# Optimization experiments

Measured on AMD Instinct MI355X. Metric: run time of the kernel, lower is better.

Reference implementation:

```python
import jax, jax.numpy as jnp
import numpy as np

B, S, D = 8, 1024, 1024
H, DH = 16, 64  # n_heads, d_head; D == H*DH


def setup_inputs() -> dict:
    key = jax.random.key(0)
    ks = jax.random.split(key, 7)
    scale = 1.0 / np.sqrt(DH)
    return {
        "images": jax.random.normal(ks[0], (B, S, D), dtype=jnp.float32),
        "Wq": jax.random.normal(ks[1], (H, DH, DH), dtype=jnp.float32) * scale,
        "bq": jax.random.normal(ks[2], (H, DH), dtype=jnp.float32) * scale,
        "Wk": jax.random.normal(ks[3], (H, DH, DH), dtype=jnp.float32) * scale,
        "bk": jax.random.normal(ks[4], (H, DH), dtype=jnp.float32) * scale,
        "Wv": jax.random.normal(ks[5], (H, DH, DH), dtype=jnp.float32) * scale,
        "bv": jax.random.normal(ks[6], (H, DH), dtype=jnp.float32) * scale,
    }


def reference(images, Wq, bq, Wk, bk, Wv, bv):
    Bn, Sn, Dn = images.shape
    x = images.reshape(Bn, Sn, H, DH)  # split hidden dim into per-head slices
    # torch Linear: y = x @ W.T + b, per head -> einsum over input dim d
    q = jnp.einsum("bshd,hod->bsho", x, Wq) + bq  # [B,S,H,DH]
    k = jnp.einsum("bshd,hod->bsho", x, Wk) + bk
    v = jnp.einsum("bshd,hod->bsho", x, Wv) + bv
    scores = jnp.einsum("bqhd,bkhd->bhqk", q, k) / jnp.sqrt(jnp.asarray(DH, x.dtype))
    attn = jax.nn.softmax(scores, axis=-1)  # [B,H,S,S]
    out = jnp.einsum("bhqk,bkhd->bqhd", attn, v)  # [B,S,H,DH]
    return out.reshape(Bn, Sn, Dn)  # hstack across heads == reshape back
```

## Files before the change

kernel.cpp:

```cpp
#include <hip/hip_runtime.h>
#include <hip/hip_bf16.h>

#define B_ 8
#define S_ 1024
#define D_ 1024
#define H_ 16
#define DH_ 64

typedef __attribute__((ext_vector_type(8))) short short8;
typedef __attribute__((ext_vector_type(8))) unsigned short ushort8;
typedef __attribute__((ext_vector_type(4))) unsigned short us4;
typedef __attribute__((ext_vector_type(4))) unsigned int uint4v;
typedef __attribute__((ext_vector_type(4))) float f32x4;

#define QSCALE 0.18033688011112042f

static __device__ __forceinline__ unsigned short f2bf(float f) {
    union { float f; unsigned u; } v; v.f = f;
    unsigned r = v.u + 0x7fffu + ((v.u >> 16) & 1u);
    return (unsigned short)(r >> 16);
}

static __device__ __forceinline__ void stage8(const float* __restrict__ src, unsigned short* dst) {
    float4 a = *reinterpret_cast<const float4*>(src);
    float4 b = *reinterpret_cast<const float4*>(src + 4);
    ushort8 r;
    r[0] = f2bf(a.x); r[1] = f2bf(a.y); r[2] = f2bf(a.z); r[3] = f2bf(a.w);
    r[4] = f2bf(b.x); r[5] = f2bf(b.y); r[6] = f2bf(b.z); r[7] = f2bf(b.w);
    *reinterpret_cast<ushort8*>(dst) = r;
}

static __device__ __forceinline__ unsigned int cvtpk(float a, float b) {
    unsigned int r;
    asm("v_cvt_pk_bf16_f32 %0, %1, %2" : "=v"(r) : "v"(a), "v"(b));
    return r;
}

__global__ __launch_bounds__(256) void qkv_proj(
    const float* __restrict__ x,
    const float* __restrict__ Wq, const float* __restrict__ bq,
    const float* __restrict__ Wk, const float* __restrict__ bk,
    const float* __restrict__ Wv, const float* __restrict__ bv,
    unsigned short* __restrict__ qo, unsigned short* __restrict__ ko,
    unsigned short* __restrict__ vo)
{
    const int bid   = blockIdx.x;
    const int stile = bid & 15;
    const int h     = (bid >> 4) & (H_ - 1);
    const int b     = bid >> 8;
    const int tid   = threadIdx.x;
    const int lane  = tid & 63;
    const int wave  = tid >> 6;
    const int lr    = lane & 15;
    const int lk    = lane >> 4;

    __shared__ __align__(16) unsigned short xs[64][72];
    __shared__ __align__(16) unsigned short wsh[3][64][72];

    {
        int row = tid >> 2;
        int col = (tid & 3) * 16;
        const float* src = x + ((size_t)(b * S_ + stile * 64 + row)) * D_ + h * DH_ + col;
        stage8(src,     &xs[row][col]);
        stage8(src + 8, &xs[row][col + 8]);
        const float* wsrc[3] = { Wq + h * DH_ * DH_, Wk + h * DH_ * DH_, Wv + h * DH_ * DH_ };
        #pragma unroll
        for (int p = 0; p < 3; ++p) {
            const float* s = wsrc[p] + row * DH_ + col;
            stage8(s,     &wsh[p][row][col]);
            stage8(s + 8, &wsh[p][row][col + 8]);
        }
    }
    __syncthreads();

    short8 a[2];
    #pragma unroll
    for (int kk = 0; kk < 2; ++kk)
        a[kk] = *reinterpret_cast<const short8*>(&xs[wave * 16 + lr][8 * lk + 32 * kk]);

    f32x4 acc[3][4];
    #pragma unroll
    for (int p = 0; p < 3; ++p)
        #pragma unroll
        for (int n = 0; n < 4; ++n)
            acc[p][n] = (f32x4){0.f, 0.f, 0.f, 0.f};

    #pragma unroll
    for (int p = 0; p < 3; ++p)
        #pragma unroll
        for (int kk = 0; kk < 2; ++kk)
            #pragma unroll
            for (int n = 0; n < 4; ++n) {
                short8 bf = *reinterpret_cast<const short8*>(&wsh[p][lr + 16 * n][8 * lk + 32 * kk]);
                acc[p][n] = __builtin_amdgcn_mfma_f32_16x16x32_bf16(a[kk], bf, acc[p][n], 0, 0, 0);
            }

    size_t base = ((size_t)(b * H_ + h) * S_ + stile * 64 + wave * 16) * DH_;
    #pragma unroll
    for (int p = 0; p < 2; ++p) {
        const float* bias = p ? (bk + h * DH_) : (bq + h * DH_);
        unsigned short* op = p ? ko : qo;
        #pragma unroll
        for (int n = 0; n < 4; ++n) {
            int col = lr + 16 * n;
            float bb = bias[col];
            #pragma unroll
            for (int r = 0; r < 4; ++r) {
                float val = acc[p][n][r] + bb;
                if (p == 0) val *= QSCALE;
                op[base + (size_t)(4 * lk + r) * DH_ + col] = f2bf(val);
            }
        }
    }
    {
        size_t vbase = (size_t)(b * H_ + h) * DH_ * S_;
        int s0 = stile * 64 + wave * 16 + 4 * lk;
        #pragma unroll
        for (int n = 0; n < 4; ++n) {
            int dh = lr + 16 * n;
            float bb = bv[h * DH_ + dh];
            us4 w;
            #pragma unroll
            for (int r = 0; r < 4; ++r) w[r] = f2bf(acc[2][n][r] + bb);
            *reinterpret_cast<us4*>(vo + vbase + (size_t)dh * S_ + s0) = w;
        }
    }
}

__global__ __launch_bounds__(256, 4) void attn_fwd(
    const unsigned short* __restrict__ q,
    const unsigned short* __restrict__ k,
    const unsigned short* __restrict__ vt,
    float* __restrict__ out)
{
    const int bid   = (blockIdx.x & 7) * 128 + (blockIdx.x >> 3);
    const int qtile = bid & 7;
    const int h     = (bid >> 3) & (H_ - 1);
    const int b     = bid >> 7;
    const int tid   = threadIdx.x;
    const int lane  = tid & 63;
    const int wave  = tid >> 6;
    const int lr    = lane & 15;
    const int lk    = lane >> 4;

    __shared__ __align__(16) unsigned short ks[2][64][64];
    __shared__ __align__(16) unsigned short vs[2][64][64];

    const size_t bh = (size_t)(b * H_ + h) * S_ * DH_;

    short8 qf[2][2];
    #pragma unroll
    for (int g = 0; g < 2; ++g) {
        const unsigned short* qp = q + bh + (size_t)(qtile * 128 + wave * 32 + 16 * g + lr) * DH_;
        #pragma unroll
        for (int kk = 0; kk < 2; ++kk)
            qf[g][kk] = *reinterpret_cast<const short8*>(qp + 8 * lk + 32 * kk);
    }

    const int srow = tid >> 2;
    const int c0   = (tid & 3) * 2;
    const int prow = (srow & 0x23) | ((srow & 4) << 2) | ((srow & 0x18) >> 1);
    const int kx   = prow & 7, vx = srow & 7;
    ushort8 kreg[2], vreg[2];

    {
        const unsigned short* srck = k + bh + (size_t)srow * DH_ + c0 * 8;
        kreg[0] = *reinterpret_cast<const ushort8*>(srck);
        kreg[1] = *reinterpret_cast<const ushort8*>(srck + 8);
        const unsigned short* srcv = vt + bh + (size_t)srow * S_ + c0 * 8;
        vreg[0] = *reinterpret_cast<const ushort8*>(srcv);
        vreg[1] = *reinterpret_cast<const ushort8*>(srcv + 8);
        *reinterpret_cast<ushort8*>(&ks[0][prow][(c0 ^ kx) * 8])       = kreg[0];
        *reinterpret_cast<ushort8*>(&ks[0][prow][((c0 + 1) ^ kx) * 8]) = kreg[1];
        *reinterpret_cast<ushort8*>(&vs[0][srow][(c0 ^ vx) * 8])       = vreg[0];
        *reinterpret_cast<ushort8*>(&vs[0][srow][((c0 + 1) ^ vx) * 8]) = vreg[1];
    }

    f32x4 acc[2][4];
    #pragma unroll
    for (int g = 0; g < 2; ++g)
        #pragma unroll
        for (int n = 0; n < 4; ++n) acc[g][n] = (f32x4){0.f, 0.f, 0.f, 0.f};
    float l0 = 0.f, l1 = 0.f;

    const int rx = lr & 7;
    const int NT = S_ / 64;
    for (int t = 0; t < NT; ++t) {
        __syncthreads();

        if (t + 1 < NT) {
            const unsigned short* srck = k + bh + (size_t)((t + 1) * 64 + srow) * DH_ + c0 * 8;
            kreg[0] = *reinterpret_cast<const ushort8*>(srck);
            kreg[1] = *reinterpret_cast<const ushort8*>(srck + 8);
            const unsigned short* srcv = vt + bh + (size_t)srow * S_ + (t + 1) * 64 + c0 * 8;
            vreg[0] = *reinterpret_cast<const ushort8*>(srcv);
            vreg[1] = *reinterpret_cast<const ushort8*>(srcv + 8);
        }
        const int cur = t & 1;

        f32x4 st[2][4];
        #pragma unroll
        for (int g = 0; g < 2; ++g)
            #pragma unroll
            for (int n = 0; n < 4; ++n) st[g][n] = (f32x4){0.f, 0.f, 0.f, 0.f};
        #pragma unroll
        for (int kk = 0; kk < 2; ++kk)
            #pragma unroll
            for (int n = 0; n < 4; ++n) {
                short8 ka = *reinterpret_cast<const short8*>(
                    &ks[cur][16 * n + lr][((lk + 4 * kk) ^ rx) * 8]);
                st[0][n] = __builtin_amdgcn_mfma_f32_16x16x32_bf16(ka, qf[0][kk], st[0][n], 0, 0, 0);
                st[1][n] = __builtin_amdgcn_mfma_f32_16x16x32_bf16(ka, qf[1][kk], st[1][n], 0, 0, 0);
            }

        #pragma unroll
        for (int g = 0; g < 2; ++g)
            #pragma unroll
            for (int n = 0; n < 4; ++n)
                #pragma unroll
                for (int r = 0; r < 4; ++r)
                    st[g][n][r] = __builtin_amdgcn_exp2f(st[g][n][r]);
        {
            float a0 = (st[0][0][0] + st[0][0][1]) + (st[0][0][2] + st[0][0][3]);
            float a1 = (st[0][1][0] + st[0][1][1]) + (st[0][1][2] + st[0][1][3]);
            float a2 = (st[0][2][0] + st[0][2][1]) + (st[0][2][2] + st[0][2][3]);
            float a3 = (st[0][3][0] + st[0][3][1]) + (st[0][3][2] + st[0][3][3]);
            l0 += (a0 + a1) + (a2 + a3);
            float b0 = (st[1][0][0] + st[1][0][1]) + (st[1][0][2] + st[1][0][3]);
            float b1 = (st[1][1][0] + st[1][1][1]) + (st[1][1][2] + st[1][1][3]);
            float b2 = (st[1][2][0] + st[1][2][1]) + (st[1][2][2] + st[1][2][3]);
            float b3 = (st[1][3][0] + st[1][3][1]) + (st[1][3][2] + st[1][3][3]);
            l1 += (b0 + b1) + (b2 + b3);
        }

        short8 pa[2][2];
        #pragma unroll
        for (int g = 0; g < 2; ++g)
            #pragma unroll
            for (int kk = 0; kk < 2; ++kk) {
                uint4v w4;
                w4[0] = cvtpk(st[g][2 * kk][0],     st[g][2 * kk][1]);
                w4[1] = cvtpk(st[g][2 * kk][2],     st[g][2 * kk][3]);
                w4[2] = cvtpk(st[g][2 * kk + 1][0], st[g][2 * kk + 1][1]);
                w4[3] = cvtpk(st[g][2 * kk + 1][2], st[g][2 * kk + 1][3]);
                pa[g][kk] = __builtin_bit_cast(short8, w4);
            }

        #pragma unroll
        for (int kk = 0; kk < 2; ++kk)
            #pragma unroll
            for (int n = 0; n < 4; ++n) {
                short8 va = *reinterpret_cast<const short8*>(
                    &vs[cur][16 * n + lr][((lk + 4 * kk) ^ rx) * 8]);
                acc[0][n] = __builtin_amdgcn_mfma_f32_16x16x32_bf16(va, pa[0][kk], acc[0][n], 0, 0, 0);
                acc[1][n] = __builtin_amdgcn_mfma_f32_16x16x32_bf16(va, pa[1][kk], acc[1][n], 0, 0, 0);
            }

        if (t + 1 < NT) {
            const int nxt = cur ^ 1;
            *reinterpret_cast<ushort8*>(&ks[nxt][prow][(c0 ^ kx) * 8])       = kreg[0];
            *reinterpret_cast<ushort8*>(&ks[nxt][prow][((c0 + 1) ^ kx) * 8]) = kreg[1];
            *reinterpret_cast<ushort8*>(&vs[nxt][srow][(c0 ^ vx) * 8])       = vreg[0];
            *reinterpret_cast<ushort8*>(&vs[nxt][srow][((c0 + 1) ^ vx) * 8]) = vreg[1];
        }
    }

    l0 += __shfl_xor(l0, 16, 64); l0 += __shfl_xor(l0, 32, 64);
    l1 += __shfl_xor(l1, 16, 64); l1 += __shfl_xor(l1, 32, 64);
    const float inv0 = 1.f / l0, inv1 = 1.f / l1;
    #pragma unroll
    for (int g = 0; g < 2; ++g) {
        const float inv = g ? inv1 : inv0;
        const int qrow = qtile * 128 + wave * 32 + 16 * g + lr;
        float* op = out + (size_t)(b * S_ + qrow) * D_ + h * DH_;
        #pragma unroll
        for (int n = 0; n < 4; ++n) {
            float4 o;
            o.x = acc[g][n][0] * inv; o.y = acc[g][n][1] * inv;
            o.z = acc[g][n][2] * inv; o.w = acc[g][n][3] * inv;
            *reinterpret_cast<float4*>(op + 16 * n + 4 * lk) = o;
        }
    }
}

extern "C" void kernel_launch(void* const* d_in, const int* in_sizes, int n_in,
                              void* d_out, int out_size, void* d_ws, size_t ws_size,
                              hipStream_t stream) {
    const float* x  = (const float*)d_in[0];
    const float* Wq = (const float*)d_in[1];
    const float* bq = (const float*)d_in[2];
    const float* Wk = (const float*)d_in[3];
    const float* bk = (const float*)d_in[4];
    const float* Wv = (const float*)d_in[5];
    const float* bv = (const float*)d_in[6];
    float* out = (float*)d_out;

    unsigned short* qw = (unsigned short*)d_ws;
    size_t per = (size_t)B_ * H_ * S_ * DH_;
    unsigned short* kw = qw + per;
    unsigned short* vw = kw + per;

    qkv_proj<<<dim3(B_ * H_ * (S_ / 64)), 256, 0, stream>>>(x, Wq, bq, Wk, bk, Wv, bv, qw, kw, vw);
    attn_fwd<<<dim3(B_ * H_ * (S_ / 128)), 256, 0, stream>>>(qw, kw, vw, out);
}
```

Baseline: 68.82 us.

## Enlarge attention query tile and stage K/V via direct global-to-LDS loads

Each attention block now processes 256 query rows, with 64 rows per wave instead of 32. Every K/V tile loaded into LDS therefore feeds twice as many MFMAs, and the grid is halved. The register-staged K/V prefetch is replaced by global_load_lds DMA into the double buffer, with the swizzle applied on the global source address rather than the LDS destination. In exchange, register pressure roughly doubles for accumulators and scores, and occupancy drops (launch bounds 256,2 with only 512 blocks), so there is less latency hiding.

```diff
diff --git a/kernel.cpp b/kernel.cpp
--- a/kernel.cpp
+++ b/kernel.cpp
@@ -34,6 +34,13 @@
     unsigned int r;
     asm("v_cvt_pk_bf16_f32 %0, %1, %2" : "=v"(r) : "v"(a), "v"(b));
     return r;
+}
+
+static __device__ __forceinline__ void gll16(const void* g, void* l) {
+    __builtin_amdgcn_global_load_lds(
+        (const __attribute__((address_space(1))) unsigned int*)g,
+        (__attribute__((address_space(3))) unsigned int*)l,
+        16, 0, 0);
 }
 
 __global__ __launch_bounds__(256) void qkv_proj(
@@ -127,16 +134,16 @@
     }
 }
 
-__global__ __launch_bounds__(256, 4) void attn_fwd(
+__global__ __launch_bounds__(256, 2) void attn_fwd(
     const unsigned short* __restrict__ q,
     const unsigned short* __restrict__ k,
     const unsigned short* __restrict__ vt,
     float* __restrict__ out)
 {
-    const int bid   = (blockIdx.x & 7) * 128 + (blockIdx.x >> 3);
-    const int qtile = bid & 7;
-    const int h     = (bid >> 3) & (H_ - 1);
-    const int b     = bid >> 7;
+    const int bid   = (blockIdx.x & 7) * 64 + (blockIdx.x >> 3);
+    const int qtile = bid & 3;
+    const int h     = (bid >> 2) & (H_ - 1);
+    const int b     = bid >> 6;
     const int tid   = threadIdx.x;
     const int lane  = tid & 63;
     const int wave  = tid >> 6;
@@ -148,59 +155,58 @@
 
     const size_t bh = (size_t)(b * H_ + h) * S_ * DH_;
 
-    short8 qf[2][2];
-    #pragma unroll
-    for (int g = 0; g < 2; ++g) {
-        const unsigned short* qp = q + bh + (size_t)(qtile * 128 + wave * 32 + 16 * g + lr) * DH_;
+    short8 qf[4][2];
+    #pragma unroll
+    for (int g = 0; g < 4; ++g) {
+        const unsigned short* qp = q + bh + (size_t)(qtile * 256 + wave * 64 + 16 * g + lr) * DH_;
         #pragma unroll
         for (int kk = 0; kk < 2; ++kk)
             qf[g][kk] = *reinterpret_cast<const short8*>(qp + 8 * lk + 32 * kk);
     }
 
-    const int srow = tid >> 2;
-    const int c0   = (tid & 3) * 2;
-    const int prow = (srow & 0x23) | ((srow & 4) << 2) | ((srow & 0x18) >> 1);
-    const int kx   = prow & 7, vx = srow & 7;
-    ushort8 kreg[2], vreg[2];
-
-    {
-        const unsigned short* srck = k + bh + (size_t)srow * DH_ + c0 * 8;
-        kreg[0] = *reinterpret_cast<const ushort8*>(srck);
-        kreg[1] = *reinterpret_cast<const ushort8*>(srck + 8);
-        const unsigned short* srcv = vt + bh + (size_t)srow * S_ + c0 * 8;
-        vreg[0] = *reinterpret_cast<const ushort8*>(srcv);
-        vreg[1] = *reinterpret_cast<const ushort8*>(srcv + 8);
-        *reinterpret_cast<ushort8*>(&ks[0][prow][(c0 ^ kx) * 8])       = kreg[0];
-        *reinterpret_cast<ushort8*>(&ks[0][prow][((c0 + 1) ^ kx) * 8]) = kreg[1];
-        *reinterpret_cast<ushort8*>(&vs[0][srow][(c0 ^ vx) * 8])       = vreg[0];
-        *reinterpret_cast<ushort8*>(&vs[0][srow][((c0 + 1) ^ vx) * 8]) = vreg[1];
-    }
-
-    f32x4 acc[2][4];
-    #pragma unroll
-    for (int g = 0; g < 2; ++g)
+    const int rp0 = 16 * wave + (lane >> 3);
+    const int rp1 = rp0 + 8;
+    const int c   = lane & 7;
+    const int gk0 = (rp0 & 0x23) | ((rp0 & 0x10) >> 2) | ((rp0 & 0x0C) << 1);
+    const int gk1 = (rp1 & 0x23) | ((rp1 & 0x10) >> 2) | ((rp1 & 0x0C) << 1);
+    const size_t kofs0 = (size_t)gk0 * DH_ + (c ^ (rp0 & 7)) * 8;
+    const size_t kofs1 = (size_t)gk1 * DH_ + (c ^ (rp1 & 7)) * 8;
+    const size_t vofs0 = (size_t)rp0 * S_ + (c ^ (rp0 & 7)) * 8;
+    const size_t vofs1 = (size_t)rp1 * S_ + (c ^ (rp1 & 7)) * 8;
+    const unsigned short* kb = k + bh;
+    const unsigned short* vb = vt + bh;
+
+    gll16(kb + kofs0, &ks[0][16 * wave][0]);
+    gll16(kb + kofs1, &ks[0][16 * wave + 8][0]);
+    gll16(vb + vofs0, &vs[0][16 * wave][0]);
+    gll16(vb + vofs1, &vs[0][16 * wave + 8][0]);
+
+    f32x4 acc[4][4];
+    #pragma unroll
+    for (int g = 0; g < 4; ++g)
         #pragma unroll
         for (int n = 0; n < 4; ++n) acc[g][n] = (f32x4){0.f, 0.f, 0.f, 0.f};
-    float l0 = 0.f, l1 = 0.f;
+    float l[4] = {0.f, 0.f, 0.f, 0.f};
 
     const int rx = lr & 7;
     const int NT = S_ / 64;
     for (int t = 0; t < NT; ++t) {
         __syncthreads();
+        const int cur = t & 1;
 
         if (t + 1 < NT) {
-            const unsigned short* srck = k + bh + (size_t)((t + 1) * 64 + srow) * DH_ + c0 * 8;
-            kreg[0] = *reinterpret_cast<const ushort8*>(srck);
-            kreg[1] = *reinterpret_cast<const ushort8*>(srck + 8);
-            const unsigned short* srcv = vt + bh + (size_t)srow * S_ + (t + 1) * 64 + c0 * 8;
-            vreg[0] = *reinterpret_cast<const ushort8*>(srcv);
-            vreg[1] = *reinterpret_cast<const ushort8*>(srcv + 8);
-        }
-        const int cur = t & 1;
-
-        f32x4 st[2][4];
-        #pragma unroll
-        for (int g = 0; g < 2; ++g)
+            const int nxt = cur ^ 1;
+            const unsigned short* kt = kb + (size_t)(t + 1) * 64 * DH_;
+            const unsigned short* vtb = vb + (size_t)(t + 1) * 64;
+            gll16(kt + kofs0, &ks[nxt][16 * wave][0]);
+            gll16(kt + kofs1, &ks[nxt][16 * wave + 8][0]);
+            gll16(vtb + vofs0, &vs[nxt][16 * wave][0]);
+            gll16(vtb + vofs1, &vs[nxt][16 * wave + 8][0]);
+        }
+
+        f32x4 st[4][4];
+        #pragma unroll
+        for (int g = 0; g < 4; ++g)
             #pragma unroll
             for (int n = 0; n < 4; ++n) st[g][n] = (f32x4){0.f, 0.f, 0.f, 0.f};
         #pragma unroll
@@ -209,33 +215,28 @@
             for (int n = 0; n < 4; ++n) {
                 short8 ka = *reinterpret_cast<const short8*>(
                     &ks[cur][16 * n + lr][((lk + 4 * kk) ^ rx) * 8]);
-                st[0][n] = __builtin_amdgcn_mfma_f32_16x16x32_bf16(ka, qf[0][kk], st[0][n], 0, 0, 0);
-                st[1][n] = __builtin_amdgcn_mfma_f32_16x16x32_bf16(ka, qf[1][kk], st[1][n], 0, 0, 0);
-            }
-
-        #pragma unroll
-        for (int g = 0; g < 2; ++g)
+                #pragma unroll
+                for (int g = 0; g < 4; ++g)
+                    st[g][n] = __builtin_amdgcn_mfma_f32_16x16x32_bf16(ka, qf[g][kk], st[g][n], 0, 0, 0);
+            }
+
+        #pragma unroll
+        for (int g = 0; g < 4; ++g) {
             #pragma unroll
             for (int n = 0; n < 4; ++n)
                 #pragma unroll
                 for (int r = 0; r < 4; ++r)
                     st[g][n][r] = __builtin_amdgcn_exp2f(st[g][n][r]);
-        {
-            float a0 = (st[0][0][0] + st[0][0][1]) + (st[0][0][2] + st[0][0][3]);
-            float a1 = (st[0][1][0] + st[0][1][1]) + (st[0][1][2] + st[0][1][3]);
-            float a2 = (st[0][2][0] + st[0][2][1]) + (st[0][2][2] + st[0][2][3]);
-            float a3 = (st[0][3][0] + st[0][3][1]) + (st[0][3][2] + st[0][3][3]);
-            l0 += (a0 + a1) + (a2 + a3);
-            float b0 = (st[1][0][0] + st[1][0][1]) + (st[1][0][2] + st[1][0][3]);
-            float b1 = (st[1][1][0] + st[1][1][1]) + (st[1][1][2] + st[1][1][3]);
-            float b2 = (st[1][2][0] + st[1][2][1]) + (st[1][2][2] + st[1][2][3]);
-            float b3 = (st[1][3][0] + st[1][3][1]) + (st[1][3][2] + st[1][3][3]);
-            l1 += (b0 + b1) + (b2 + b3);
-        }
-
-        short8 pa[2][2];
-        #pragma unroll
-        for (int g = 0; g < 2; ++g)
+            float a0 = (st[g][0][0] + st[g][0][1]) + (st[g][0][2] + st[g][0][3]);
+            float a1 = (st[g][1][0] + st[g][1][1]) + (st[g][1][2] + st[g][1][3]);
+            float a2 = (st[g][2][0] + st[g][2][1]) + (st[g][2][2] + st[g][2][3]);
+            float a3 = (st[g][3][0] + st[g][3][1]) + (st[g][3][2] + st[g][3][3]);
+            l[g] += (a0 + a1) + (a2 + a3);
+        }
+
+        short8 pa[4][2];
+        #pragma unroll
+        for (int g = 0; g < 4; ++g)
             #pragma unroll
             for (int kk = 0; kk < 2; ++kk) {
                 uint4v w4;
@@ -252,26 +253,19 @@
             for (int n = 0; n < 4; ++n) {
                 short8 va = *reinterpret_cast<const short8*>(
                     &vs[cur][16 * n + lr][((lk + 4 * kk) ^ rx) * 8]);
-                acc[0][n] = __builtin_amdgcn_mfma_f32_16x16x32_bf16(va, pa[0][kk], acc[0][n], 0, 0, 0);
-                acc[1][n] = __builtin_amdgcn_mfma_f32_16x16x32_bf16(va, pa[1][kk], acc[1][n], 0, 0, 0);
-            }
-
-        if (t + 1 < NT) {
-            const int nxt = cur ^ 1;
-            *reinterpret_cast<ushort8*>(&ks[nxt][prow][(c0 ^ kx) * 8])       = kreg[0];
-            *reinterpret_cast<ushort8*>(&ks[nxt][prow][((c0 + 1) ^ kx) * 8]) = kreg[1];
-            *reinterpret_cast<ushort8*>(&vs[nxt][srow][(c0 ^ vx) * 8])       = vreg[0];
-            *reinterpret_cast<ushort8*>(&vs[nxt][srow][((c0 + 1) ^ vx) * 8]) = vreg[1];
-        }
-    }
-
-    l0 += __shfl_xor(l0, 16, 64); l0 += __shfl_xor(l0, 32, 64);
-    l1 += __shfl_xor(l1, 16, 64); l1 += __shfl_xor(l1, 32, 64);
-    const float inv0 = 1.f / l0, inv1 = 1.f / l1;
-    #pragma unroll
-    for (int g = 0; g < 2; ++g) {
-        const float inv = g ? inv1 : inv0;
-        const int qrow = qtile * 128 + wave * 32 + 16 * g + lr;
+                #pragma unroll
+                for (int g = 0; g < 4; ++g)
+                    acc[g][n] = __builtin_amdgcn_mfma_f32_16x16x32_bf16(va, pa[g][kk], acc[g][n], 0, 0, 0);
+            }
+    }
+
+    #pragma unroll
+    for (int g = 0; g < 4; ++g) {
+        float lg = l[g];
+        lg += __shfl_xor(lg, 16, 64);
+        lg += __shfl_xor(lg, 32, 64);
+        const float inv = 1.f / lg;
+        const int qrow = qtile * 256 + wave * 64 + 16 * g + lr;
         float* op = out + (size_t)(b * S_ + qrow) * D_ + h * DH_;
         #pragma unroll
         for (int n = 0; n < 4; ++n) {
@@ -301,5 +295,5 @@
     unsigned short* vw = kw + per;
 
     qkv_proj<<<dim3(B_ * H_ * (S_ / 64)), 256, 0, stream>>>(x, Wq, bq, Wk, bk, Wv, bv, qw, kw, vw);
-    attn_fwd<<<dim3(B_ * H_ * (S_ / 128)), 256, 0, stream>>>(qw, kw, vw, out);
-}
+    attn_fwd<<<dim3(B_ * H_ * (S_ / 256)), 256, 0, stream>>>(qw, kw, vw, out);
+}
```

Result: faster. 66.60 us (-3.2%).

## Stage K/V tiles via global_load_lds with 128-key tiles

Applied to the files above, without the earlier changes.

Replaces the register-staged global-to-LDS copy of K and V tiles with direct global_load_lds DMA, applying the XOR swizzle on the global side. It also doubles the key tile from 64 to 128, which halves the number of loop iterations and barriers. Launch bounds drop to 2 blocks per CU because LDS and register use grow. The intent is to remove VGPR staging and LDS store instructions and to overlap the next tile's load with compute. The cost is lower occupancy and a prefetch that has no explicit wait before the barrier, which could be a correctness risk.

```diff
diff --git a/kernel.cpp b/kernel.cpp
--- a/kernel.cpp
+++ b/kernel.cpp
@@ -34,6 +34,13 @@
     unsigned int r;
     asm("v_cvt_pk_bf16_f32 %0, %1, %2" : "=v"(r) : "v"(a), "v"(b));
     return r;
+}
+
+static __device__ __forceinline__ void gll16(const void* g, void* l) {
+    __builtin_amdgcn_global_load_lds(
+        (const __attribute__((address_space(1))) unsigned int*)g,
+        (__attribute__((address_space(3))) unsigned int*)l,
+        16, 0, 0);
 }
 
 __global__ __launch_bounds__(256) void qkv_proj(
@@ -127,7 +134,7 @@
     }
 }
 
-__global__ __launch_bounds__(256, 4) void attn_fwd(
+__global__ __launch_bounds__(256, 2) void attn_fwd(
     const unsigned short* __restrict__ q,
     const unsigned short* __restrict__ k,
     const unsigned short* __restrict__ vt,
@@ -143,8 +150,8 @@
     const int lr    = lane & 15;
     const int lk    = lane >> 4;
 
-    __shared__ __align__(16) unsigned short ks[2][64][64];
-    __shared__ __align__(16) unsigned short vs[2][64][64];
+    __shared__ __align__(16) unsigned short ks[2][128][64];
+    __shared__ __align__(16) unsigned short vs[2][64][128];
 
     const size_t bh = (size_t)(b * H_ + h) * S_ * DH_;
 
@@ -157,23 +164,22 @@
             qf[g][kk] = *reinterpret_cast<const short8*>(qp + 8 * lk + 32 * kk);
     }
 
-    const int srow = tid >> 2;
-    const int c0   = (tid & 3) * 2;
-    const int prow = (srow & 0x23) | ((srow & 4) << 2) | ((srow & 0x18) >> 1);
-    const int kx   = prow & 7, vx = srow & 7;
-    ushort8 kreg[2], vreg[2];
-
-    {
-        const unsigned short* srck = k + bh + (size_t)srow * DH_ + c0 * 8;
-        kreg[0] = *reinterpret_cast<const ushort8*>(srck);
-        kreg[1] = *reinterpret_cast<const ushort8*>(srck + 8);
-        const unsigned short* srcv = vt + bh + (size_t)srow * S_ + c0 * 8;
-        vreg[0] = *reinterpret_cast<const ushort8*>(srcv);
-        vreg[1] = *reinterpret_cast<const ushort8*>(srcv + 8);
-        *reinterpret_cast<ushort8*>(&ks[0][prow][(c0 ^ kx) * 8])       = kreg[0];
-        *reinterpret_cast<ushort8*>(&ks[0][prow][((c0 + 1) ^ kx) * 8]) = kreg[1];
-        *reinterpret_cast<ushort8*>(&vs[0][srow][(c0 ^ vx) * 8])       = vreg[0];
-        *reinterpret_cast<ushort8*>(&vs[0][srow][((c0 + 1) ^ vx) * 8]) = vreg[1];
+    size_t kofs[4], vofs[4];
+    #pragma unroll
+    for (int j = 0; j < 4; ++j) {
+        const int rp = 32 * wave + 8 * j + (lane >> 3);
+        const int gk = (rp & 0x63) | ((rp & 0x10) >> 2) | ((rp & 0x0C) << 1);
+        kofs[j] = (size_t)gk * DH_ + (size_t)(((lane & 7) ^ (rp & 7)) * 8);
+        const int rv = 16 * wave + 4 * j + (lane >> 4);
+        vofs[j] = (size_t)rv * S_ + (size_t)(((lane & 15) ^ (rv & 15)) * 8);
+    }
+    const unsigned short* kb = k + bh;
+    const unsigned short* vb = vt + bh;
+
+    #pragma unroll
+    for (int j = 0; j < 4; ++j) {
+        gll16(kb + kofs[j], &ks[0][32 * wave + 8 * j][0]);
+        gll16(vb + vofs[j], &vs[0][16 * wave + 4 * j][0]);
     }
 
     f32x4 acc[2][4];
@@ -181,32 +187,34 @@
     for (int g = 0; g < 2; ++g)
         #pragma unroll
         for (int n = 0; n < 4; ++n) acc[g][n] = (f32x4){0.f, 0.f, 0.f, 0.f};
-    float l0 = 0.f, l1 = 0.f;
+    float l[2] = {0.f, 0.f};
 
     const int rx = lr & 7;
-    const int NT = S_ / 64;
+    const int NT = S_ / 128;
     for (int t = 0; t < NT; ++t) {
         __syncthreads();
+        const int cur = t & 1;
 
         if (t + 1 < NT) {
-            const unsigned short* srck = k + bh + (size_t)((t + 1) * 64 + srow) * DH_ + c0 * 8;
-            kreg[0] = *reinterpret_cast<const ushort8*>(srck);
-            kreg[1] = *reinterpret_cast<const ushort8*>(srck + 8);
-            const unsigned short* srcv = vt + bh + (size_t)srow * S_ + (t + 1) * 64 + c0 * 8;
-            vreg[0] = *reinterpret_cast<const ushort8*>(srcv);
-            vreg[1] = *reinterpret_cast<const ushort8*>(srcv + 8);
-        }
-        const int cur = t & 1;
-
-        f32x4 st[2][4];
+            const int nxt = cur ^ 1;
+            const unsigned short* kt  = kb + (size_t)(t + 1) * 128 * DH_;
+            const unsigned short* vtb = vb + (size_t)(t + 1) * 128;
+            #pragma unroll
+            for (int j = 0; j < 4; ++j) {
+                gll16(kt + kofs[j],  &ks[nxt][32 * wave + 8 * j][0]);
+                gll16(vtb + vofs[j], &vs[nxt][16 * wave + 4 * j][0]);
+            }
+        }
+
+        f32x4 st[2][8];
         #pragma unroll
         for (int g = 0; g < 2; ++g)
             #pragma unroll
-            for (int n = 0; n < 4; ++n) st[g][n] = (f32x4){0.f, 0.f, 0.f, 0.f};
+            for (int n = 0; n < 8; ++n) st[g][n] = (f32x4){0.f, 0.f, 0.f, 0.f};
         #pragma unroll
         for (int kk = 0; kk < 2; ++kk)
             #pragma unroll
-            for (int n = 0; n < 4; ++n) {
+            for (int n = 0; n < 8; ++n) {
                 short8 ka = *reinterpret_cast<const short8*>(
                     &ks[cur][16 * n + lr][((lk + 4 * kk) ^ rx) * 8]);
                 st[0][n] = __builtin_amdgcn_mfma_f32_16x16x32_bf16(ka, qf[0][kk], st[0][n], 0, 0, 0);
@@ -214,30 +222,26 @@
             }
 
         #pragma unroll
-        for (int g = 0; g < 2; ++g)
-            #pragma unroll
-            for (int n = 0; n < 4; ++n)
+        for (int g = 0; g < 2; ++g) {
+            #pragma unroll
+            for (int n = 0; n < 8; ++n)
                 #pragma unroll
                 for (int r = 0; r < 4; ++r)
                     st[g][n][r] = __builtin_amdgcn_exp2f(st[g][n][r]);
-        {
-            float a0 = (st[0][0][0] + st[0][0][1]) + (st[0][0][2] + st[0][0][3]);
-            float a1 = (st[0][1][0] + st[0][1][1]) + (st[0][1][2] + st[0][1][3]);
-            float a2 = (st[0][2][0] + st[0][2][1]) + (st[0][2][2] + st[0][2][3]);
-            float a3 = (st[0][3][0] + st[0][3][1]) + (st[0][3][2] + st[0][3][3]);
-            l0 += (a0 + a1) + (a2 + a3);
-            float b0 = (st[1][0][0] + st[1][0][1]) + (st[1][0][2] + st[1][0][3]);
-            float b1 = (st[1][1][0] + st[1][1][1]) + (st[1][1][2] + st[1][1][3]);
-            float b2 = (st[1][2][0] + st[1][2][1]) + (st[1][2][2] + st[1][2][3]);
-            float b3 = (st[1][3][0] + st[1][3][1]) + (st[1][3][2] + st[1][3][3]);
-            l1 += (b0 + b1) + (b2 + b3);
-        }
-
-        short8 pa[2][2];
+            float s0 = 0.f, s1 = 0.f;
+            #pragma unroll
+            for (int n = 0; n < 4; ++n) {
+                s0 += (st[g][n][0] + st[g][n][1]) + (st[g][n][2] + st[g][n][3]);
+                s1 += (st[g][n + 4][0] + st[g][n + 4][1]) + (st[g][n + 4][2] + st[g][n + 4][3]);
+            }
+            l[g] += s0 + s1;
+        }
+
+        short8 pa[2][4];
         #pragma unroll
         for (int g = 0; g < 2; ++g)
             #pragma unroll
-            for (int kk = 0; kk < 2; ++kk) {
+            for (int kk = 0; kk < 4; ++kk) {
                 uint4v w4;
                 w4[0] = cvtpk(st[g][2 * kk][0],     st[g][2 * kk][1]);
                 w4[1] = cvtpk(st[g][2 * kk][2],     st[g][2 * kk][3]);
@@ -247,30 +251,22 @@
             }
 
         #pragma unroll
-        for (int kk = 0; kk < 2; ++kk)
+        for (int kk = 0; kk < 4; ++kk)
             #pragma unroll
             for (int n = 0; n < 4; ++n) {
                 short8 va = *reinterpret_cast<const short8*>(
-                    &vs[cur][16 * n + lr][((lk + 4 * kk) ^ rx) * 8]);
+                    &vs[cur][16 * n + lr][((lk + 4 * kk) ^ lr) * 8]);
                 acc[0][n] = __builtin_amdgcn_mfma_f32_16x16x32_bf16(va, pa[0][kk], acc[0][n], 0, 0, 0);
                 acc[1][n] = __builtin_amdgcn_mfma_f32_16x16x32_bf16(va, pa[1][kk], acc[1][n], 0, 0, 0);
             }
-
-        if (t + 1 < NT) {
-            const int nxt = cur ^ 1;
-            *reinterpret_cast<ushort8*>(&ks[nxt][prow][(c0 ^ kx) * 8])       = kreg[0];
-            *reinterpret_cast<ushort8*>(&ks[nxt][prow][((c0 + 1) ^ kx) * 8]) = kreg[1];
-            *reinterpret_cast<ushort8*>(&vs[nxt][srow][(c0 ^ vx) * 8])       = vreg[0];
-            *reinterpret_cast<ushort8*>(&vs[nxt][srow][((c0 + 1) ^ vx) * 8]) = vreg[1];
-        }
-    }
-
-    l0 += __shfl_xor(l0, 16, 64); l0 += __shfl_xor(l0, 32, 64);
-    l1 += __shfl_xor(l1, 16, 64); l1 += __shfl_xor(l1, 32, 64);
-    const float inv0 = 1.f / l0, inv1 = 1.f / l1;
+    }
+
     #pragma unroll
     for (int g = 0; g < 2; ++g) {
-        const float inv = g ? inv1 : inv0;
+        float lg = l[g];
+        lg += __shfl_xor(lg, 16, 64);
+        lg += __shfl_xor(lg, 32, 64);
+        const float inv = 1.f / lg;
         const int qrow = qtile * 128 + wave * 32 + 16 * g + lr;
         float* op = out + (size_t)(b * S_ + qrow) * D_ + h * DH_;
         #pragma unroll
```

Result: no change. 68.33 us (-0.7%).
